# Optimization experiments

Hardware: AMD Instinct MI355X
Metric: run time of the kernel (lower is better)

Reference implementation:

```python
import jax, jax.numpy as jnp
import numpy as np

N_NODES = 50000
N_EDGES = 800000
IN_DIM = 128
HGC = 128
LG = 3
K = 3
N_CLASSES = 10
BN_EPS = 1e-5


def setup_inputs() -> dict:
    key = jax.random.key(0)
    ks = jax.random.split(key, 16)
    inp = {
        "features": jax.random.normal(ks[0], (N_NODES, IN_DIM), dtype=jnp.float32),
        "edge_index": jax.random.randint(ks[1], (2, N_EDGES), 0, N_NODES, dtype=jnp.int64),
        "edge_weight": jax.random.uniform(ks[2], (N_EDGES,), dtype=jnp.float32),
    }
    # ChebConv weights: one (K, in, out) stack per layer (PyG: K separate bias-free Linears)
    dims = [IN_DIM] + [HGC] * LG
    for i in range(LG):
        fan_in = dims[i]
        inp[f"W{i}"] = jax.random.normal(ks[3 + i], (K, dims[i], dims[i + 1]), dtype=jnp.float32) * np.sqrt(2.0 / fan_in)
    # classifier head: Linear(HGC,256) -> ReLU -> BatchNorm1d(256) -> Linear(256, num_classes)
    inp["Wc1"] = jax.random.normal(ks[8], (HGC, 256), dtype=jnp.float32) * np.sqrt(2.0 / HGC)
    inp["bc1"] = jnp.zeros((256,), dtype=jnp.float32)
    inp["gamma"] = jnp.ones((256,), dtype=jnp.float32)
    inp["beta"] = jnp.zeros((256,), dtype=jnp.float32)
    inp["Wc2"] = jax.random.normal(ks[9], (256, N_CLASSES), dtype=jnp.float32) * np.sqrt(2.0 / 256)
    inp["bc2"] = jnp.zeros((N_CLASSES,), dtype=jnp.float32)
    return inp


def _scaled_laplacian_weights(edge_index, edge_weight, n_nodes):
    # get_laplacian(sym): L = I - D^{-1/2} A D^{-1/2}; ChebConv scales 2L/lambda_max - I
    # with lambda_max = 2.0 -> L_hat off-diagonal weights = -A_norm, diagonal = 0.
    row, col = edge_index[0], edge_index[1]
    deg = jax.ops.segment_sum(edge_weight, row, num_segments=n_nodes)
    dinv = jnp.where(deg > 0, jax.lax.rsqrt(jnp.maximum(deg, 1e-30)), 0.0)
    return -dinv[row] * edge_weight * dinv[col]


def _propagate(x, row, col, w, n_nodes):
    # SpMM: (L_hat @ x)[i] = sum_e w[e] * x[col[e]] for row[e]==i
    return jax.ops.segment_sum(w[:, None] * x[col], row, num_segments=n_nodes)


def _cheb_conv(x, W, row, col, w, n_nodes):
    # W: (K, in, out). Chebyshev recursion T0=x, T1=Lx, Tk=2LT_{k-1}-T_{k-2}
    Tx0 = x
    out = Tx0 @ W[0]
    Tx1 = _propagate(Tx0, row, col, w, n_nodes)
    out = out + Tx1 @ W[1]
    for k in range(2, W.shape[0]):
        Tx2 = 2.0 * _propagate(Tx1, row, col, w, n_nodes) - Tx0
        out = out + Tx2 @ W[k]
        Tx0, Tx1 = Tx1, Tx2
    return out


def reference(features, edge_index, edge_weight, W0, W1, W2, Wc1, bc1, gamma, beta, Wc2, bc2):
    n = features.shape[0]
    row, col = edge_index[0], edge_index[1]
    w = _scaled_laplacian_weights(edge_index, edge_weight, n)
    x = features
    for W in (W0, W1, W2):
        x = jax.nn.relu(_cheb_conv(x, W, row, col, w, n))  # dropout is identity in eval
    h = jax.nn.relu(x @ Wc1 + bc1)
    mean = jnp.mean(h, axis=0)
    var = jnp.var(h, axis=0)  # biased, as torch BatchNorm1d normalization
    h = (h - mean) * jax.lax.rsqrt(var + BN_EPS) * gamma + beta
    logit = h @ Wc2 + bc2
    return (logit, edge_weight)
```

## Files before the change

kernel.cpp:

```cpp
#include <hip/hip_runtime.h>
#include <cstdint>
#include <cstddef>

#define DIM 128
#define BN_EPS 1e-5f
#define NS 8
#define CHUNK_SHIFT 13
#define FIX_SCALE 16777216.0f

typedef short bf16x8 __attribute__((ext_vector_type(8)));
typedef float f32x4 __attribute__((ext_vector_type(4)));

__device__ __forceinline__ unsigned short f2bf(float f) {
  unsigned u = __float_as_uint(f);
  u = (u + 0x7fffu + ((u >> 16) & 1u)) >> 16;
  return (unsigned short)u;
}
__device__ __forceinline__ float bf2f(unsigned v) {
  return __uint_as_float(v << 16);
}


__global__ void deg_hist_kernel(const int* __restrict__ ei, const float* __restrict__ ew,
                                unsigned long long* __restrict__ pck,
                                unsigned* __restrict__ eidx, int E, int N) {
  int e = blockIdx.x * blockDim.x + threadIdx.x;
  if (e < E) {
    int r = ei[e];
    int g = ei[E + e] >> CHUNK_SHIFT;
    unsigned fix = (unsigned)(ew[e] * FIX_SCALE + 0.5f);
    unsigned long long old =
        atomicAdd(&pck[(size_t)g * N + r], (1ull << 32) | (unsigned long long)fix);
    eidx[e] = (unsigned)(old >> 32);
  }
}

__global__ void reduce_dinv_kernel(const unsigned long long* __restrict__ pck,
                                   float* __restrict__ dinv, int N) {
  int i = blockIdx.x * blockDim.x + threadIdx.x;
  if (i < N) {
    float d = 0.f;
#pragma unroll
    for (int g = 0; g < NS; ++g)
      d += (float)(unsigned)(pck[(size_t)g * N + i] & 0xffffffffull);
    d *= (1.0f / FIX_SCALE);
    dinv[i] = d > 0.f ? rsqrtf(fmaxf(d, 1e-30f)) : 0.f;
  }
}

__global__ __launch_bounds__(512) void scan_a_kernel(const unsigned long long* __restrict__ pck,
                                                     int* __restrict__ off2,
                                                     int* __restrict__ bsums, int n8, int N) {
  __shared__ int sd[512];
  int t = threadIdx.x;
  int i = blockIdx.x * 512 + t;
  int v = 0;
  if (i < n8) {
    int g = i & (NS - 1), r = i >> 3;
    v = (int)(pck[(size_t)g * N + r] >> 32);
  }
  sd[t] = v;
  __syncthreads();
  for (int off = 1; off < 512; off <<= 1) {
    int x = (t >= off) ? sd[t - off] : 0;
    __syncthreads();
    sd[t] += x;
    __syncthreads();
  }
  if (i < n8) off2[i] = sd[t] - v;
  if (t == 511) bsums[blockIdx.x] = sd[511];
}

__global__ __launch_bounds__(1024) void scan_b_kernel(int* __restrict__ bsums, int nb) {
  __shared__ int sd[1024];
  int t = threadIdx.x;
  int v = (t < nb) ? bsums[t] : 0;
  sd[t] = v;
  __syncthreads();
  for (int off = 1; off < 1024; off <<= 1) {
    int x = (t >= off) ? sd[t - off] : 0;
    __syncthreads();
    sd[t] += x;
    __syncthreads();
  }
  if (t < nb) bsums[t] = sd[t] - v;
}

__global__ __launch_bounds__(512) void scan_c_kernel(int* __restrict__ off2,
                                                     const int* __restrict__ bsums,
                                                     int* __restrict__ row_ptr, int n8, int N,
                                                     int E) {
  int i = blockIdx.x * 512 + threadIdx.x;
  if (i < n8) {
    int v = off2[i] + bsums[blockIdx.x];
    off2[i] = v;
    if ((i & (NS - 1)) == 0) row_ptr[i >> 3] = v;
  }
  if (blockIdx.x == 0 && threadIdx.x == 0) row_ptr[N] = E;
}

__global__ void scatter_kernel(const int* __restrict__ ei, const float* __restrict__ ew,
                               const float* __restrict__ dinv, const int* __restrict__ off2,
                               const unsigned* __restrict__ eidx, int2* __restrict__ cw, int E,
                               int N) {
  int e = blockIdx.x * blockDim.x + threadIdx.x;
  if (e < E) {
    int r = ei[e], c = ei[E + e];
    int g = c >> CHUNK_SHIFT;
    float w = -dinv[r] * ew[e] * dinv[c];
    int pos = off2[r * NS + g] + (int)eidx[e];
    cw[pos] = make_int2(c, __float_as_int(w));
  }
}


__global__ void combine_weightsT_kernel(const float* __restrict__ W0,
                                        const float* __restrict__ W1,
                                        const float* __restrict__ W2,
                                        unsigned short* __restrict__ WcatT) {
  int l = blockIdx.y;
  const float* W = (l == 0) ? W0 : (l == 1) ? W1 : W2;
  unsigned short* outp = WcatT + (size_t)l * 128 * 384;
  int idx = blockIdx.x * blockDim.x + threadIdx.x;
  if (idx < DIM * DIM) {
    int i = idx >> 7, o = idx & 127;
    float w0 = W[i * DIM + o];
    float w1 = W[DIM * DIM + i * DIM + o];
    float w2 = W[2 * DIM * DIM + i * DIM + o];
    outp[(size_t)o * 384 + i] = f2bf(w0 - w2);
    outp[(size_t)o * 384 + 128 + i] = f2bf(w1);
    outp[(size_t)o * 384 + 256 + i] = f2bf(2.0f * w2);
  }
}

__global__ void wc1t_kernel(const float* __restrict__ Wc1, unsigned short* __restrict__ Wc1T) {
  int idx = blockIdx.x * blockDim.x + threadIdx.x;
  if (idx < 128 * 256) {
    int k = idx >> 8, n = idx & 255;
    Wc1T[(size_t)n * 128 + k] = f2bf(Wc1[(size_t)k * 256 + n]);
  }
}

__global__ void f2bf_kernel(const float* __restrict__ in, unsigned short* __restrict__ outp,
                            int n4) {
  int i = blockIdx.x * blockDim.x + threadIdx.x;
  if (i < n4) {
    float4 v = reinterpret_cast<const float4*>(in)[i];
    ushort4 o;
    o.x = f2bf(v.x); o.y = f2bf(v.y); o.z = f2bf(v.z); o.w = f2bf(v.w);
    reinterpret_cast<ushort4*>(outp)[i] = o;
  }
}


__global__ __launch_bounds__(256) void spmm_kernel(const int* __restrict__ row_ptr,
                                                   const int2* __restrict__ cw,
                                                   const unsigned short* __restrict__ X,
                                                   unsigned short* __restrict__ Y, int N) {
  int row = (blockIdx.x * blockDim.x + threadIdx.x) >> 6;
  int lane = threadIdx.x & 63;
  if (row >= N) return;
  int half = lane >> 5;
  int l32 = lane & 31;
  int cb = l32 * 4;
  int s = row_ptr[row], e = row_ptr[row + 1];
  float a0 = 0.f, a1 = 0.f, a2 = 0.f, a3 = 0.f;
  float b0 = 0.f, b1 = 0.f, b2 = 0.f, b3 = 0.f;
  int j = s + half;
  for (; j + 6 < e; j += 8) {
    int2 e0 = cw[j], e1 = cw[j + 2], e2 = cw[j + 4], e3 = cw[j + 6];
    uint2 v0 = *reinterpret_cast<const uint2*>(X + (size_t)e0.x * DIM + cb);
    uint2 v1 = *reinterpret_cast<const uint2*>(X + (size_t)e1.x * DIM + cb);
    uint2 v2 = *reinterpret_cast<const uint2*>(X + (size_t)e2.x * DIM + cb);
    uint2 v3 = *reinterpret_cast<const uint2*>(X + (size_t)e3.x * DIM + cb);
    float w0 = __int_as_float(e0.y), w1 = __int_as_float(e1.y);
    float w2 = __int_as_float(e2.y), w3 = __int_as_float(e3.y);
    a0 += w0 * bf2f(v0.x & 0xffffu); a1 += w0 * bf2f(v0.x >> 16);
    a2 += w0 * bf2f(v0.y & 0xffffu); a3 += w0 * bf2f(v0.y >> 16);
    b0 += w1 * bf2f(v1.x & 0xffffu); b1 += w1 * bf2f(v1.x >> 16);
    b2 += w1 * bf2f(v1.y & 0xffffu); b3 += w1 * bf2f(v1.y >> 16);
    a0 += w2 * bf2f(v2.x & 0xffffu); a1 += w2 * bf2f(v2.x >> 16);
    a2 += w2 * bf2f(v2.y & 0xffffu); a3 += w2 * bf2f(v2.y >> 16);
    b0 += w3 * bf2f(v3.x & 0xffffu); b1 += w3 * bf2f(v3.x >> 16);
    b2 += w3 * bf2f(v3.y & 0xffffu); b3 += w3 * bf2f(v3.y >> 16);
  }
  for (; j < e; j += 2) {
    int2 e0 = cw[j];
    uint2 v0 = *reinterpret_cast<const uint2*>(X + (size_t)e0.x * DIM + cb);
    float w0 = __int_as_float(e0.y);
    a0 += w0 * bf2f(v0.x & 0xffffu); a1 += w0 * bf2f(v0.x >> 16);
    a2 += w0 * bf2f(v0.y & 0xffffu); a3 += w0 * bf2f(v0.y >> 16);
  }
  a0 += b0; a1 += b1; a2 += b2; a3 += b3;
  a0 += __shfl_xor(a0, 32);
  a1 += __shfl_xor(a1, 32);
  a2 += __shfl_xor(a2, 32);
  a3 += __shfl_xor(a3, 32);
  if (half == 0) {
    uint2 o;
    o.x = (unsigned)f2bf(a0) | ((unsigned)f2bf(a1) << 16);
    o.y = (unsigned)f2bf(a2) | ((unsigned)f2bf(a3) << 16);
    *reinterpret_cast<uint2*>(Y + (size_t)row * DIM + cb) = o;
  }
}


__global__ __launch_bounds__(256) void gemm3_mfma_kernel(const unsigned short* __restrict__ X,
                                                         const unsigned short* __restrict__ S1,
                                                         const unsigned short* __restrict__ S2,
                                                         const unsigned short* __restrict__ BT,
                                                         unsigned short* __restrict__ out, int M) {
  __shared__ short As[128 * 40];
  __shared__ short Bs[128 * 40];
  int tid = threadIdx.x;
  int wv = tid >> 6, ln = tid & 63;
  int lg = ln >> 4, lr = ln & 15;
  int blockRow = blockIdx.x * 128;
  f32x4 acc[2][8];
#pragma unroll
  for (int m = 0; m < 2; ++m)
#pragma unroll
    for (int n = 0; n < 8; ++n) acc[m][n] = (f32x4){0.f, 0.f, 0.f, 0.f};
  const unsigned short* srcs[3] = {X, S1, S2};
  int srow = tid >> 1;
  int scol = (tid & 1) * 16;
  int arow = blockRow + srow;
  bool aok = arow < M;
  for (int seg = 0; seg < 3; ++seg) {
    const unsigned short* src = srcs[seg];
    for (int k0 = 0; k0 < DIM; k0 += 32) {
      float4 av0, av1;
      if (aok) {
        const float4* ap = reinterpret_cast<const float4*>(src + (size_t)arow * DIM + k0 + scol);
        av0 = ap[0];
        av1 = ap[1];
      } else {
        av0 = make_float4(0.f, 0.f, 0.f, 0.f);
        av1 = av0;
      }
      const float4* bp =
          reinterpret_cast<const float4*>(BT + (size_t)srow * 384 + seg * DIM + k0 + scol);
      float4 bv0 = bp[0], bv1 = bp[1];
      __syncthreads();
      *reinterpret_cast<float4*>(&As[srow * 40 + scol]) = av0;
      *reinterpret_cast<float4*>(&As[srow * 40 + scol + 8]) = av1;
      *reinterpret_cast<float4*>(&Bs[srow * 40 + scol]) = bv0;
      *reinterpret_cast<float4*>(&Bs[srow * 40 + scol + 8]) = bv1;
      __syncthreads();
      bf16x8 af[2], bf[8];
#pragma unroll
      for (int m = 0; m < 2; ++m)
        af[m] = *reinterpret_cast<const bf16x8*>(&As[(wv * 32 + m * 16 + lr) * 40 + lg * 8]);
#pragma unroll
      for (int n = 0; n < 8; ++n)
        bf[n] = *reinterpret_cast<const bf16x8*>(&Bs[(n * 16 + lr) * 40 + lg * 8]);
#pragma unroll
      for (int m = 0; m < 2; ++m)
#pragma unroll
        for (int n = 0; n < 8; ++n)
          acc[m][n] = __builtin_amdgcn_mfma_f32_16x16x32_bf16(af[m], bf[n], acc[m][n], 0, 0, 0);
    }
  }
#pragma unroll
  for (int m = 0; m < 2; ++m)
#pragma unroll
    for (int n = 0; n < 8; ++n) {
      int col = n * 16 + lr;
#pragma unroll
      for (int r = 0; r < 4; ++r) {
        int grow = blockRow + wv * 32 + m * 16 + lg * 4 + r;
        if (grow < M) out[(size_t)grow * DIM + col] = f2bf(fmaxf(acc[m][n][r], 0.f));
      }
    }
}


__global__ __launch_bounds__(256) void head_mfma_kernel(const unsigned short* __restrict__ X,
                                                        const unsigned short* __restrict__ BT,
                                                        const float* __restrict__ bc1,
                                                        unsigned short* __restrict__ h,
                                                        float* __restrict__ sums, int M) {
  __shared__ short As[128 * 40];
  __shared__ short Bs[128 * 40];
  int tid = threadIdx.x;
  int wv = tid >> 6, ln = tid & 63;
  int lg = ln >> 4, lr = ln & 15;
  int blockRow = blockIdx.x * 128;
  int n0 = blockIdx.y * 128;
  f32x4 acc[2][8];
#pragma unroll
  for (int m = 0; m < 2; ++m)
#pragma unroll
    for (int n = 0; n < 8; ++n) acc[m][n] = (f32x4){0.f, 0.f, 0.f, 0.f};
  int srow = tid >> 1;
  int scol = (tid & 1) * 16;
  int arow = blockRow + srow;
  bool aok = arow < M;
  for (int k0 = 0; k0 < DIM; k0 += 32) {
    float4 av0, av1;
    if (aok) {
      const float4* ap = reinterpret_cast<const float4*>(X + (size_t)arow * DIM + k0 + scol);
      av0 = ap[0];
      av1 = ap[1];
    } else {
      av0 = make_float4(0.f, 0.f, 0.f, 0.f);
      av1 = av0;
    }
    const float4* bp =
        reinterpret_cast<const float4*>(BT + (size_t)(n0 + srow) * DIM + k0 + scol);
    float4 bv0 = bp[0], bv1 = bp[1];
    __syncthreads();
    *reinterpret_cast<float4*>(&As[srow * 40 + scol]) = av0;
    *reinterpret_cast<float4*>(&As[srow * 40 + scol + 8]) = av1;
    *reinterpret_cast<float4*>(&Bs[srow * 40 + scol]) = bv0;
    *reinterpret_cast<float4*>(&Bs[srow * 40 + scol + 8]) = bv1;
    __syncthreads();
    bf16x8 af[2], bf[8];
#pragma unroll
    for (int m = 0; m < 2; ++m)
      af[m] = *reinterpret_cast<const bf16x8*>(&As[(wv * 32 + m * 16 + lr) * 40 + lg * 8]);
#pragma unroll
    for (int n = 0; n < 8; ++n)
      bf[n] = *reinterpret_cast<const bf16x8*>(&Bs[(n * 16 + lr) * 40 + lg * 8]);
#pragma unroll
    for (int m = 0; m < 2; ++m)
#pragma unroll
      for (int n = 0; n < 8; ++n)
        acc[m][n] = __builtin_amdgcn_mfma_f32_16x16x32_bf16(af[m], bf[n], acc[m][n], 0, 0, 0);
  }
  float psum[8], psq[8];
#pragma unroll
  for (int n = 0; n < 8; ++n) { psum[n] = 0.f; psq[n] = 0.f; }
#pragma unroll
  for (int m = 0; m < 2; ++m)
#pragma unroll
    for (int n = 0; n < 8; ++n) {
      int colg = n0 + n * 16 + lr;
      float bias = bc1[colg];
#pragma unroll
      for (int r = 0; r < 4; ++r) {
        int grow = blockRow + wv * 32 + m * 16 + lg * 4 + r;
        if (grow < M) {
          float v = fmaxf(acc[m][n][r] + bias, 0.f);
          h[(size_t)grow * 256 + colg] = f2bf(v);
          psum[n] += v;
          psq[n] += v * v;
        }
      }
    }
  float* Rs = reinterpret_cast<float*>(As);
  int rid = wv * 4 + lg;
  __syncthreads();
#pragma unroll
  for (int n = 0; n < 8; ++n) Rs[rid * 128 + n * 16 + lr] = psum[n];
  __syncthreads();
  if (tid < 128) {
    float s = 0.f;
#pragma unroll
    for (int r = 0; r < 16; ++r) s += Rs[r * 128 + tid];
    atomicAdd(&sums[n0 + tid], s);
  }
  __syncthreads();
#pragma unroll
  for (int n = 0; n < 8; ++n) Rs[rid * 128 + n * 16 + lr] = psq[n];
  __syncthreads();
  if (tid < 128) {
    float s = 0.f;
#pragma unroll
    for (int r = 0; r < 16; ++r) s += Rs[r * 128 + tid];
    atomicAdd(&sums[256 + n0 + tid], s);
  }
}

__global__ __launch_bounds__(256) void bnfold_kernel(const float* __restrict__ sums,
                                                     const float* __restrict__ gamma,
                                                     const float* __restrict__ beta,
                                                     const float* __restrict__ Wc2,
                                                     const float* __restrict__ bc2,
                                                     float* __restrict__ W2e,
                                                     float* __restrict__ b2e, int M) {
  __shared__ float bsh[256];
  int c = threadIdx.x;
  float mean = sums[c] / (float)M;
  float var = sums[256 + c] / (float)M - mean * mean;
  float a = gamma[c] * rsqrtf(var + BN_EPS);
  float b = beta[c] - mean * a;
  for (int j = 0; j < 10; ++j) W2e[c * 10 + j] = a * Wc2[c * 10 + j];
  bsh[c] = b;
  __syncthreads();
  if (c < 10) {
    float t = bc2[c];
    for (int k = 0; k < 256; ++k) t += bsh[k] * Wc2[k * 10 + c];
    b2e[c] = t;
  }
}


__global__ __launch_bounds__(256) void final_kernel(const unsigned short* __restrict__ h,
                                                    const float* __restrict__ W2e,
                                                    const float* __restrict__ b2e,
                                                    float* __restrict__ out, int M) {
  __shared__ float Ws[2560];
  __shared__ float bs[16];
  for (int i = threadIdx.x; i < 2560; i += 256) Ws[i] = W2e[i];
  if (threadIdx.x < 10) bs[threadIdx.x] = b2e[threadIdx.x];
  __syncthreads();
  int row = blockIdx.x * 256 + threadIdx.x;
  if (row >= M) return;
  float p[10];
#pragma unroll
  for (int j = 0; j < 10; ++j) p[j] = bs[j];
  const uint4* hp = reinterpret_cast<const uint4*>(h + (size_t)row * 256);
#pragma unroll 4
  for (int k0 = 0; k0 < 32; ++k0) {
    uint4 v = hp[k0];
    unsigned vv[4] = {v.x, v.y, v.z, v.w};
#pragma unroll
    for (int t = 0; t < 4; ++t) {
      float f0 = bf2f(vv[t] & 0xffffu);
      float f1 = bf2f(vv[t] >> 16);
      const float* w0 = &Ws[(k0 * 8 + t * 2) * 10];
#pragma unroll
      for (int j = 0; j < 10; ++j) p[j] += f0 * w0[j] + f1 * w0[10 + j];
    }
  }
#pragma unroll
  for (int j = 0; j < 10; ++j) out[(size_t)row * 10 + j] = p[j];
}

__global__ void copy4_kernel(const float* __restrict__ src, float* __restrict__ dst, int n) {
  int i = blockIdx.x * blockDim.x + threadIdx.x;
  int i4 = i * 4;
  if (i4 + 3 < n) {
    reinterpret_cast<float4*>(dst)[i] = reinterpret_cast<const float4*>(src)[i];
  } else {
    for (int k = i4; k < n; ++k) dst[k] = src[k];
  }
}


extern "C" void kernel_launch(void* const* d_in, const int* in_sizes, int n_in,
                              void* d_out, int out_size, void* d_ws, size_t ws_size,
                              hipStream_t stream) {
  const float* features = (const float*)d_in[0];
  const int* ei = (const int*)d_in[1];
  const float* ew = (const float*)d_in[2];
  const float* W0 = (const float*)d_in[3];
  const float* W1 = (const float*)d_in[4];
  const float* W2 = (const float*)d_in[5];
  const float* Wc1 = (const float*)d_in[6];
  const float* bc1 = (const float*)d_in[7];
  const float* gamma = (const float*)d_in[8];
  const float* beta = (const float*)d_in[9];
  const float* Wc2 = (const float*)d_in[10];
  const float* bc2 = (const float*)d_in[11];
  float* out = (float*)d_out;

  const int N = in_sizes[0] / DIM;
  const int E = in_sizes[2];
  const int n8 = N * NS;

  size_t off = 0;
  auto alloc = [&](size_t bytes) -> void* {
    void* p = (char*)d_ws + off;
    off += (bytes + 511) & ~(size_t)511;
    return p;
  };
  float* dinv = (float*)alloc((size_t)N * 4);
  unsigned long long* pck = (unsigned long long*)alloc((size_t)n8 * 8);
  unsigned* eidx = (unsigned*)alloc((size_t)E * 4);
  int* off2 = (int*)alloc((size_t)(n8 + NS) * 4);
  int* bsums = (int*)alloc(1024 * 4);
  int* row_ptr = (int*)alloc((size_t)(N + 1) * 4);
  int2* cw = (int2*)alloc((size_t)E * 8);
  unsigned short* featbf = (unsigned short*)alloc((size_t)N * DIM * 2);
  unsigned short* xbuf = (unsigned short*)alloc((size_t)N * DIM * 2);
  unsigned short* S1 = (unsigned short*)alloc((size_t)N * DIM * 2);
  unsigned short* S2 = (unsigned short*)alloc((size_t)N * DIM * 2);
  unsigned short* h = (unsigned short*)alloc((size_t)N * 256 * 2);
  unsigned short* WcatT = (unsigned short*)alloc((size_t)3 * 128 * 384 * 2);
  unsigned short* Wc1T = (unsigned short*)alloc((size_t)256 * 128 * 2);
  float* W2e = (float*)alloc(2560 * 4);
  float* b2e = (float*)alloc(16 * 4);
  float* sums = (float*)alloc(512 * 4);

  hipMemsetAsync(pck, 0, (size_t)n8 * 8, stream);
  hipMemsetAsync(sums, 0, 512 * 4, stream);

  int eb = (E + 255) / 256;
  int nb = (N + 255) / 256;
  int sa_blocks = (n8 + 511) / 512;

  f2bf_kernel<<<(N * DIM / 4 + 255) / 256, 256, 0, stream>>>(features, featbf, N * DIM / 4);
  deg_hist_kernel<<<eb, 256, 0, stream>>>(ei, ew, pck, eidx, E, N);
  reduce_dinv_kernel<<<nb, 256, 0, stream>>>(pck, dinv, N);
  scan_a_kernel<<<sa_blocks, 512, 0, stream>>>(pck, off2, bsums, n8, N);
  scan_b_kernel<<<1, 1024, 0, stream>>>(bsums, sa_blocks);
  scan_c_kernel<<<sa_blocks, 512, 0, stream>>>(off2, bsums, row_ptr, n8, N, E);
  scatter_kernel<<<eb, 256, 0, stream>>>(ei, ew, dinv, off2, eidx, cw, E, N);

  dim3 cwgrid((DIM * DIM + 255) / 256, 3);
  combine_weightsT_kernel<<<cwgrid, 256, 0, stream>>>(W0, W1, W2, WcatT);
  wc1t_kernel<<<(128 * 256 + 255) / 256, 256, 0, stream>>>(Wc1, Wc1T);

  int spmm_blocks = (N + 3) / 4;
  int gemm_blocks = (N + 127) / 128;
  for (int l = 0; l < 3; ++l) {
    const unsigned short* X = (l == 0) ? featbf : xbuf;
    spmm_kernel<<<spmm_blocks, 256, 0, stream>>>(row_ptr, cw, X, S1, N);
    spmm_kernel<<<spmm_blocks, 256, 0, stream>>>(row_ptr, cw, S1, S2, N);
    gemm3_mfma_kernel<<<gemm_blocks, 256, 0, stream>>>(X, S1, S2, WcatT + (size_t)l * 128 * 384,
                                                       xbuf, N);
  }

  dim3 hgrid(gemm_blocks, 2);
  head_mfma_kernel<<<hgrid, 256, 0, stream>>>(xbuf, Wc1T, bc1, h, sums, N);
  bnfold_kernel<<<1, 256, 0, stream>>>(sums, gamma, beta, Wc2, bc2, W2e, b2e, N);
  final_kernel<<<(N + 255) / 256, 256, 0, stream>>>(h, W2e, b2e, out, N);
  copy4_kernel<<<(E / 4 + 255) / 256, 256, 0, stream>>>(ew, out + (size_t)N * 10, E);
}
```

Measured before the change: 405.8 us.

## Split SpMM into two feature-half passes with four edge groups per row

```diff
diff --git a/kernel.cpp b/kernel.cpp
--- a/kernel.cpp
+++ b/kernel.cpp
@@ -153,38 +153,31 @@
 }
 
 
-__global__ __launch_bounds__(256) void spmm_kernel(const int* __restrict__ row_ptr,
-                                                   const int2* __restrict__ cw,
-                                                   const unsigned short* __restrict__ X,
-                                                   unsigned short* __restrict__ Y, int N) {
+__global__ __launch_bounds__(256) void spmm_slice_kernel(const int* __restrict__ row_ptr,
+                                                         const int2* __restrict__ cw,
+                                                         const unsigned short* __restrict__ X,
+                                                         unsigned short* __restrict__ Y, int N,
+                                                         int foff) {
   int row = (blockIdx.x * blockDim.x + threadIdx.x) >> 6;
   int lane = threadIdx.x & 63;
   if (row >= N) return;
-  int half = lane >> 5;
-  int l32 = lane & 31;
-  int cb = l32 * 4;
+  int grp = lane >> 4;
+  int cb = foff + (lane & 15) * 4;
   int s = row_ptr[row], e = row_ptr[row + 1];
   float a0 = 0.f, a1 = 0.f, a2 = 0.f, a3 = 0.f;
   float b0 = 0.f, b1 = 0.f, b2 = 0.f, b3 = 0.f;
-  int j = s + half;
-  for (; j + 6 < e; j += 8) {
-    int2 e0 = cw[j], e1 = cw[j + 2], e2 = cw[j + 4], e3 = cw[j + 6];
+  int j = s + grp;
+  for (; j + 4 < e; j += 8) {
+    int2 e0 = cw[j], e1 = cw[j + 4];
     uint2 v0 = *reinterpret_cast<const uint2*>(X + (size_t)e0.x * DIM + cb);
     uint2 v1 = *reinterpret_cast<const uint2*>(X + (size_t)e1.x * DIM + cb);
-    uint2 v2 = *reinterpret_cast<const uint2*>(X + (size_t)e2.x * DIM + cb);
-    uint2 v3 = *reinterpret_cast<const uint2*>(X + (size_t)e3.x * DIM + cb);
     float w0 = __int_as_float(e0.y), w1 = __int_as_float(e1.y);
-    float w2 = __int_as_float(e2.y), w3 = __int_as_float(e3.y);
     a0 += w0 * bf2f(v0.x & 0xffffu); a1 += w0 * bf2f(v0.x >> 16);
     a2 += w0 * bf2f(v0.y & 0xffffu); a3 += w0 * bf2f(v0.y >> 16);
     b0 += w1 * bf2f(v1.x & 0xffffu); b1 += w1 * bf2f(v1.x >> 16);
     b2 += w1 * bf2f(v1.y & 0xffffu); b3 += w1 * bf2f(v1.y >> 16);
-    a0 += w2 * bf2f(v2.x & 0xffffu); a1 += w2 * bf2f(v2.x >> 16);
-    a2 += w2 * bf2f(v2.y & 0xffffu); a3 += w2 * bf2f(v2.y >> 16);
-    b0 += w3 * bf2f(v3.x & 0xffffu); b1 += w3 * bf2f(v3.x >> 16);
-    b2 += w3 * bf2f(v3.y & 0xffffu); b3 += w3 * bf2f(v3.y >> 16);
-  }
-  for (; j < e; j += 2) {
+  }
+  if (j < e) {
     int2 e0 = cw[j];
     uint2 v0 = *reinterpret_cast<const uint2*>(X + (size_t)e0.x * DIM + cb);
     float w0 = __int_as_float(e0.y);
@@ -192,11 +185,11 @@
     a2 += w0 * bf2f(v0.y & 0xffffu); a3 += w0 * bf2f(v0.y >> 16);
   }
   a0 += b0; a1 += b1; a2 += b2; a3 += b3;
-  a0 += __shfl_xor(a0, 32);
-  a1 += __shfl_xor(a1, 32);
-  a2 += __shfl_xor(a2, 32);
-  a3 += __shfl_xor(a3, 32);
-  if (half == 0) {
+  a0 += __shfl_xor(a0, 16); a1 += __shfl_xor(a1, 16);
+  a2 += __shfl_xor(a2, 16); a3 += __shfl_xor(a3, 16);
+  a0 += __shfl_xor(a0, 32); a1 += __shfl_xor(a1, 32);
+  a2 += __shfl_xor(a2, 32); a3 += __shfl_xor(a3, 32);
+  if (grp == 0) {
     uint2 o;
     o.x = (unsigned)f2bf(a0) | ((unsigned)f2bf(a1) << 16);
     o.y = (unsigned)f2bf(a2) | ((unsigned)f2bf(a3) << 16);
@@ -507,8 +500,10 @@
   int gemm_blocks = (N + 127) / 128;
   for (int l = 0; l < 3; ++l) {
     const unsigned short* X = (l == 0) ? featbf : xbuf;
-    spmm_kernel<<<spmm_blocks, 256, 0, stream>>>(row_ptr, cw, X, S1, N);
-    spmm_kernel<<<spmm_blocks, 256, 0, stream>>>(row_ptr, cw, S1, S2, N);
+    spmm_slice_kernel<<<spmm_blocks, 256, 0, stream>>>(row_ptr, cw, X, S1, N, 0);
+    spmm_slice_kernel<<<spmm_blocks, 256, 0, stream>>>(row_ptr, cw, X, S1, N, 64);
+    spmm_slice_kernel<<<spmm_blocks, 256, 0, stream>>>(row_ptr, cw, S1, S2, N, 0);
+    spmm_slice_kernel<<<spmm_blocks, 256, 0, stream>>>(row_ptr, cw, S1, S2, N, 64);
     gemm3_mfma_kernel<<<gemm_blocks, 256, 0, stream>>>(X, S1, S2, WcatT + (size_t)l * 128 * 384,
                                                        xbuf, N);
   }
```

Result: slower. 484.6 us (+19.4%).
